# Kernel optimization log

Measured on AMD Instinct MI355X. Metric: run time of the kernel, lower is better.

The kernel has to match this reference:

```python
import jax, jax.numpy as jnp
import numpy as np

LATENT = 3
POLY = 3
SINDY_DIM = 22  # 3 ones + 3 linear + 6 quad + 10 cubic


def sindy_library(z, poly_order=POLY, latent_dim=LATENT):
    # z: [N, latent_dim] -> [N, sindy_dim]; mirrors the torch loop ordering.
    N = z.shape[0]
    cols = [jnp.ones((N,), z.dtype) for _ in range(latent_dim)]
    if poly_order > 0:
        cols += [z[:, i] for i in range(latent_dim)]
    if poly_order > 1:
        for i in range(latent_dim):
            for j in range(i, latent_dim):
                cols.append(z[:, i] * z[:, j])
    if poly_order > 2:
        for i in range(latent_dim):
            for j in range(i, latent_dim):
                for k in range(j, latent_dim):
                    cols.append(z[:, i] * z[:, j] * z[:, k])
    return jnp.stack(cols, axis=1)


def _xavier(key, out_f, in_f):
    lim = np.sqrt(6.0 / (in_f + out_f)).astype(np.float32)
    return jax.random.uniform(key, (out_f, in_f), jnp.float32, -lim, lim)


def setup_inputs() -> dict:
    key = jax.random.key(0)
    ks = jax.random.split(key, 16)
    N, D = 262144, 128
    we = [128, 64, 32, 3]
    wd = [3, 32, 64, 128]
    d = {}
    d["x"] = jax.random.normal(ks[0], (N, D), jnp.float32)
    d["dx"] = jax.random.normal(ks[1], (N, D), jnp.float32)
    for li, (i_f, o_f) in enumerate(zip(we[:-1], we[1:])):
        d[f"We{li+1}"] = _xavier(ks[2 + li], o_f, i_f)
        d[f"be{li+1}"] = jnp.zeros((o_f,), jnp.float32)
    for li, (i_f, o_f) in enumerate(zip(wd[:-1], wd[1:])):
        d[f"Wd{li+1}"] = _xavier(ks[6 + li], o_f, i_f)
        d[f"bd{li+1}"] = jnp.zeros((o_f,), jnp.float32)
    d["EW"] = jnp.full((LATENT, SINDY_DIM), 0.5, jnp.float32)  # nn.init.constant_(E.weight, 0.5)
    d["Eb"] = jax.random.normal(ks[10], (LATENT,), jnp.float32) * 0.1
    return d


def reference(x, dx, We1, be1, We2, be2, We3, be3,
              Wd1, bd1, Wd2, bd2, Wd3, bd3, EW, Eb):
    # encoder forward (Linear + Identity chain)
    z = ((x @ We1.T + be1) @ We2.T + be2) @ We3.T + be3            # [N, L]
    # encoder Jacobian is constant (pure linear chain): J_enc = We3 @ We2 @ We1
    J_enc = We3 @ We2 @ We1                                        # [L, D]
    dz = dx @ J_enc.T                                              # [N, L]
    # SINDy prediction of z-dot
    theta = sindy_library(z)                                       # [N, SINDY_DIM]
    dzb = theta @ EW.T + Eb                                        # [N, L]
    # decoder forward
    xb = ((z @ Wd1.T + bd1) @ Wd2.T + bd2) @ Wd3.T + bd3           # [N, D]
    # decoder Jacobian (constant)
    J_dec = Wd3 @ Wd2 @ Wd1                                        # [D, L]
    dxb = dzb @ J_dec.T                                            # [N, D]
    return z, dz, dzb, xb, dxb
```

## Files before the change

kernel.cpp:

```cpp
#include <hip/hip_runtime.h>

#define D 128

typedef float f32x4 __attribute__((ext_vector_type(4)));

__device__ __forceinline__ float dpp_half_sum(float v) {
    #define DPP_STEP(ctrl, rowmask)                                           \
        v += __int_as_float(__builtin_amdgcn_update_dpp(                      \
                 0, __float_as_int(v), (ctrl), (rowmask), 0xF, true))
    DPP_STEP(0x111, 0xF);
    DPP_STEP(0x112, 0xF);
    DPP_STEP(0x114, 0xF);
    DPP_STEP(0x118, 0xF);
    DPP_STEP(0x142, 0xA);
    #undef DPP_STEP
    return v;
}

__global__ __launch_bounds__(256) void fuse_weights(
    const float* __restrict__ We1, const float* __restrict__ be1,
    const float* __restrict__ We2, const float* __restrict__ be2,
    const float* __restrict__ We3, const float* __restrict__ be3,
    const float* __restrict__ Wd1, const float* __restrict__ bd1,
    const float* __restrict__ Wd2, const float* __restrict__ bd2,
    const float* __restrict__ Wd3, const float* __restrict__ bd3,
    float* __restrict__ ws)
{
    __shared__ float A1[3][64];
    __shared__ float B1[64][3];
    __shared__ float t2d[64];
    const int t = threadIdx.x;

    if (t < 192) {
        {   int r = t >> 6, c = t & 63;
            float s = 0.f;
            #pragma unroll 8
            for (int i = 0; i < 32; ++i) s += We3[r * 32 + i] * We2[i * 64 + c];
            A1[r][c] = s;
        }
        {   int o = t / 3, l = t - o * 3;
            float s = 0.f;
            #pragma unroll 8
            for (int i = 0; i < 32; ++i) s += Wd2[o * 32 + i] * Wd1[i * 3 + l];
            B1[o][l] = s;
        }
    } else {
        int i = t - 192;
        float s = bd2[i];
        #pragma unroll 8
        for (int j = 0; j < 32; ++j) s += Wd2[i * 32 + j] * bd1[j];
        t2d[i] = s;
    }
    __syncthreads();

    for (int e = t; e < 3 * D; e += 256) {
        int r = e >> 7, c = e & 127;
        float s = 0.f;
        #pragma unroll 8
        for (int j = 0; j < 64; ++j) s += A1[r][j] * We1[j * D + c];
        ws[e] = s;
    }
    if (t < 3) {
        float s = be3[t];
        #pragma unroll 8
        for (int j = 0; j < 64; ++j) s += A1[t][j] * be1[j];
        #pragma unroll 8
        for (int i = 0; i < 32; ++i) s += We3[t * 32 + i] * be2[i];
        ws[384 + t] = s;
    }
    if (t < 128) {
        float s0 = 0.f, s1 = 0.f, s2 = 0.f, sb = bd3[t];
        #pragma unroll 8
        for (int j = 0; j < 64; ++j) {
            float w = Wd3[t * 64 + j];
            s0 += w * B1[j][0];
            s1 += w * B1[j][1];
            s2 += w * B1[j][2];
            sb += w * t2d[j];
        }
        ws[512 + t * 4 + 0] = s0;
        ws[512 + t * 4 + 1] = s1;
        ws[512 + t * 4 + 2] = s2;
        ws[512 + t * 4 + 3] = sb;
    }
}

__global__ __launch_bounds__(256) void sindy_all(
    const float* __restrict__ x, const float* __restrict__ dx,
    const float* __restrict__ EW, const float* __restrict__ Eb,
    const float* __restrict__ ws, float* __restrict__ out, int nrows)
{
    __shared__ float sz[768];
    __shared__ float sdz[768];
    __shared__ float sdzb[768];
    __shared__ float sew[69];

    const int t    = threadIdx.x;
    const int lane = t & 31;
    const int half = t >> 5;

    if (t < 66) sew[t] = EW[t];
    else if (t < 69) sew[t] = Eb[t - 66];

    const f32x4 je0 = *((const f32x4*)(ws +   0) + lane);
    const f32x4 je1 = *((const f32x4*)(ws + 128) + lane);
    const f32x4 je2 = *((const f32x4*)(ws + 256) + lane);
    const float benc0 = ws[384], benc1 = ws[385], benc2 = ws[386];
    const f32x4 jd0 = *((const f32x4*)(ws + 512) + lane * 4 + 0);
    const f32x4 jd1 = *((const f32x4*)(ws + 512) + lane * 4 + 1);
    const f32x4 jd2 = *((const f32x4*)(ws + 512) + lane * 4 + 2);
    const f32x4 jd3 = *((const f32x4*)(ws + 512) + lane * 4 + 3);

    const int base = blockIdx.x * 256;
    const int rem  = nrows - base;

    #pragma unroll 4
    for (int i = 0; i < 32; ++i) {
        const int r2  = i * 8 + half;
        const int row = base + r2;
        if (row >= nrows) continue;
        const f32x4 xv = __builtin_nontemporal_load((const f32x4*)(x + (size_t)row * D) + lane);
        float z0 = je0.x*xv.x + je0.y*xv.y + je0.z*xv.z + je0.w*xv.w;
        float z1 = je1.x*xv.x + je1.y*xv.y + je1.z*xv.z + je1.w*xv.w;
        float z2 = je2.x*xv.x + je2.y*xv.y + je2.z*xv.z + je2.w*xv.w;
        z0 = dpp_half_sum(z0);
        z1 = dpp_half_sum(z1);
        z2 = dpp_half_sum(z2);
        if (lane == 31) {
            sz[r2 * 3 + 0] = z0 + benc0;
            sz[r2 * 3 + 1] = z1 + benc1;
            sz[r2 * 3 + 2] = z2 + benc2;
        }
    }

    #pragma unroll 4
    for (int i = 0; i < 32; ++i) {
        const int r2  = i * 8 + half;
        const int row = base + r2;
        if (row >= nrows) continue;
        const f32x4 dv = __builtin_nontemporal_load((const f32x4*)(dx + (size_t)row * D) + lane);
        float d0 = je0.x*dv.x + je0.y*dv.y + je0.z*dv.z + je0.w*dv.w;
        float d1 = je1.x*dv.x + je1.y*dv.y + je1.z*dv.z + je1.w*dv.w;
        float d2 = je2.x*dv.x + je2.y*dv.y + je2.z*dv.z + je2.w*dv.w;
        d0 = dpp_half_sum(d0);
        d1 = dpp_half_sum(d1);
        d2 = dpp_half_sum(d2);
        if (lane == 31) {
            sdz[r2 * 3 + 0] = d0;
            sdz[r2 * 3 + 1] = d1;
            sdz[r2 * 3 + 2] = d2;
        }
    }

    __syncthreads();

    if (t < rem) {
        const float z0 = sz[t * 3 + 0];
        const float z1 = sz[t * 3 + 1];
        const float z2 = sz[t * 3 + 2];

        const float q00 = z0*z0, q01 = z0*z1, q02 = z0*z2;
        const float q11 = z1*z1, q12 = z1*z2, q22 = z2*z2;
        float th[19];
        th[0]=z0;  th[1]=z1;  th[2]=z2;
        th[3]=q00; th[4]=q01; th[5]=q02; th[6]=q11; th[7]=q12; th[8]=q22;
        th[9]=q00*z0;  th[10]=q00*z1; th[11]=q00*z2;
        th[12]=q11*z0; th[13]=q12*z0; th[14]=q22*z0;
        th[15]=q11*z1; th[16]=q11*z2; th[17]=q22*z1; th[18]=q22*z2;

        float b0 = sew[66] + sew[0]  + sew[1]  + sew[2];
        float b1 = sew[67] + sew[22] + sew[23] + sew[24];
        float b2 = sew[68] + sew[44] + sew[45] + sew[46];
        #pragma unroll
        for (int k = 0; k < 19; ++k) {
            b0 += sew[3  + k] * th[k];
            b1 += sew[25 + k] * th[k];
            b2 += sew[47 + k] * th[k];
        }
        sdzb[t * 3 + 0] = b0;
        sdzb[t * 3 + 1] = b1;
        sdzb[t * 3 + 2] = b2;
    }

    __syncthreads();

    if (rem >= 256) {
        if (t < 192) {
            ((f32x4*)(out + (size_t)base * 3))[t]                     = ((const f32x4*)sz)[t];
            ((f32x4*)(out + 3 * (size_t)nrows + (size_t)base * 3))[t] = ((const f32x4*)sdz)[t];
            ((f32x4*)(out + 6 * (size_t)nrows + (size_t)base * 3))[t] = ((const f32x4*)sdzb)[t];
        }
    } else {
        for (int e = t; e < rem * 3; e += 256) {
            out[(size_t)base * 3 + e]                     = sz[e];
            out[3 * (size_t)nrows + (size_t)base * 3 + e] = sdz[e];
            out[6 * (size_t)nrows + (size_t)base * 3 + e] = sdzb[e];
        }
    }

    float* __restrict__ xbout = out + 9 * (size_t)nrows;
    #pragma unroll 4
    for (int i = 0; i < 32; ++i) {
        const int r2  = i * 8 + half;
        const int row = base + r2;
        if (row >= nrows) continue;
        const float z0 = sz[r2 * 3 + 0];
        const float z1 = sz[r2 * 3 + 1];
        const float z2 = sz[r2 * 3 + 2];
        f32x4 v;
        v.x = jd0.x*z0 + jd0.y*z1 + jd0.z*z2 + jd0.w;
        v.y = jd1.x*z0 + jd1.y*z1 + jd1.z*z2 + jd1.w;
        v.z = jd2.x*z0 + jd2.y*z1 + jd2.z*z2 + jd2.w;
        v.w = jd3.x*z0 + jd3.y*z1 + jd3.z*z2 + jd3.w;
        __builtin_nontemporal_store(v, (f32x4*)(xbout + (size_t)row * D) + lane);
    }

    float* __restrict__ dxbout = out + 137 * (size_t)nrows;
    #pragma unroll 4
    for (int i = 0; i < 32; ++i) {
        const int r2  = i * 8 + half;
        const int row = base + r2;
        if (row >= nrows) continue;
        const float b0 = sdzb[r2 * 3 + 0];
        const float b1 = sdzb[r2 * 3 + 1];
        const float b2 = sdzb[r2 * 3 + 2];
        f32x4 v;
        v.x = jd0.x*b0 + jd0.y*b1 + jd0.z*b2;
        v.y = jd1.x*b0 + jd1.y*b1 + jd1.z*b2;
        v.z = jd2.x*b0 + jd2.y*b1 + jd2.z*b2;
        v.w = jd3.x*b0 + jd3.y*b1 + jd3.z*b2;
        __builtin_nontemporal_store(v, (f32x4*)(dxbout + (size_t)row * D) + lane);
    }
}

extern "C" void kernel_launch(void* const* d_in, const int* in_sizes, int n_in,
                              void* d_out, int out_size, void* d_ws, size_t ws_size,
                              hipStream_t stream) {
    const float* x   = (const float*)d_in[0];
    const float* dx  = (const float*)d_in[1];
    const float* We1 = (const float*)d_in[2];
    const float* be1 = (const float*)d_in[3];
    const float* We2 = (const float*)d_in[4];
    const float* be2 = (const float*)d_in[5];
    const float* We3 = (const float*)d_in[6];
    const float* be3 = (const float*)d_in[7];
    const float* Wd1 = (const float*)d_in[8];
    const float* bd1 = (const float*)d_in[9];
    const float* Wd2 = (const float*)d_in[10];
    const float* bd2 = (const float*)d_in[11];
    const float* Wd3 = (const float*)d_in[12];
    const float* bd3 = (const float*)d_in[13];
    const float* EW  = (const float*)d_in[14];
    const float* Eb  = (const float*)d_in[15];

    float* ws  = (float*)d_ws;
    float* out = (float*)d_out;
    const int nrows = in_sizes[0] / D;
    const int nblk  = (nrows + 255) / 256;

    fuse_weights<<<1, 256, 0, stream>>>(We1, be1, We2, be2, We3, be3,
                                        Wd1, bd1, Wd2, bd2, Wd3, bd3, ws);

    sindy_all<<<nblk, 256, 0, stream>>>(x, dx, EW, Eb, ws, out, nrows);
}
```

Measured before the change: 112.8 us.

## Fold weight-fusion kernel into main kernel and drop nontemporal memory hints

Removes the separate single-block fuse_weights launch. Every block of sindy_all now recomputes the fused encoder/decoder Jacobians and biases into shared memory, which avoids one kernel launch and the serialization gap between the two launches. In exchange, each of the 1024 blocks does redundant weight math and reads from the weight arrays (mostly L2 hits) before starting its streaming work. Loads and stores of x, dx, xb and dxb also switch from nontemporal builtins to plain vector accesses.

```diff
diff --git a/kernel.cpp b/kernel.cpp
--- a/kernel.cpp
+++ b/kernel.cpp
@@ -17,99 +17,97 @@
     return v;
 }
 
-__global__ __launch_bounds__(256) void fuse_weights(
+__global__ __launch_bounds__(256) void sindy_all(
+    const float* __restrict__ x, const float* __restrict__ dx,
     const float* __restrict__ We1, const float* __restrict__ be1,
     const float* __restrict__ We2, const float* __restrict__ be2,
     const float* __restrict__ We3, const float* __restrict__ be3,
     const float* __restrict__ Wd1, const float* __restrict__ bd1,
     const float* __restrict__ Wd2, const float* __restrict__ bd2,
     const float* __restrict__ Wd3, const float* __restrict__ bd3,
-    float* __restrict__ ws)
+    const float* __restrict__ EW, const float* __restrict__ Eb,
+    float* __restrict__ out, int nrows)
 {
-    __shared__ float A1[3][64];
-    __shared__ float B1[64][3];
-    __shared__ float t2d[64];
-    const int t = threadIdx.x;
+    __shared__ alignas(16) float A1s[192];
+    __shared__ alignas(16) float B1s[192];
+    __shared__ alignas(16) float t2ds[64];
+    __shared__ alignas(16) float sje[384];
+    __shared__ alignas(16) float sjd[512];
+    __shared__ alignas(16) float sbenc[3];
+    __shared__ alignas(16) float sew[69];
+    __shared__ alignas(16) float sz[768];
+    __shared__ alignas(16) float sdz[768];
+    __shared__ alignas(16) float sdzb[768];
+
+    const int t    = threadIdx.x;
+    const int lane = t & 31;
+    const int half = t >> 5;
 
     if (t < 192) {
         {   int r = t >> 6, c = t & 63;
             float s = 0.f;
             #pragma unroll 8
             for (int i = 0; i < 32; ++i) s += We3[r * 32 + i] * We2[i * 64 + c];
-            A1[r][c] = s;
+            A1s[r * 64 + c] = s;
         }
         {   int o = t / 3, l = t - o * 3;
             float s = 0.f;
             #pragma unroll 8
             for (int i = 0; i < 32; ++i) s += Wd2[o * 32 + i] * Wd1[i * 3 + l];
-            B1[o][l] = s;
+            B1s[o * 3 + l] = s;
         }
     } else {
         int i = t - 192;
         float s = bd2[i];
         #pragma unroll 8
         for (int j = 0; j < 32; ++j) s += Wd2[i * 32 + j] * bd1[j];
-        t2d[i] = s;
-    }
-    __syncthreads();
-
-    for (int e = t; e < 3 * D; e += 256) {
-        int r = e >> 7, c = e & 127;
-        float s = 0.f;
-        #pragma unroll 8
-        for (int j = 0; j < 64; ++j) s += A1[r][j] * We1[j * D + c];
-        ws[e] = s;
-    }
-    if (t < 3) {
-        float s = be3[t];
-        #pragma unroll 8
-        for (int j = 0; j < 64; ++j) s += A1[t][j] * be1[j];
-        #pragma unroll 8
-        for (int i = 0; i < 32; ++i) s += We3[t * 32 + i] * be2[i];
-        ws[384 + t] = s;
-    }
-    if (t < 128) {
-        float s0 = 0.f, s1 = 0.f, s2 = 0.f, sb = bd3[t];
-        #pragma unroll 8
-        for (int j = 0; j < 64; ++j) {
-            float w = Wd3[t * 64 + j];
-            s0 += w * B1[j][0];
-            s1 += w * B1[j][1];
-            s2 += w * B1[j][2];
-            sb += w * t2d[j];
-        }
-        ws[512 + t * 4 + 0] = s0;
-        ws[512 + t * 4 + 1] = s1;
-        ws[512 + t * 4 + 2] = s2;
-        ws[512 + t * 4 + 3] = sb;
-    }
-}
-
-__global__ __launch_bounds__(256) void sindy_all(
-    const float* __restrict__ x, const float* __restrict__ dx,
-    const float* __restrict__ EW, const float* __restrict__ Eb,
-    const float* __restrict__ ws, float* __restrict__ out, int nrows)
-{
-    __shared__ float sz[768];
-    __shared__ float sdz[768];
-    __shared__ float sdzb[768];
-    __shared__ float sew[69];
-
-    const int t    = threadIdx.x;
-    const int lane = t & 31;
-    const int half = t >> 5;
-
-    if (t < 66) sew[t] = EW[t];
-    else if (t < 69) sew[t] = Eb[t - 66];
-
-    const f32x4 je0 = *((const f32x4*)(ws +   0) + lane);
-    const f32x4 je1 = *((const f32x4*)(ws + 128) + lane);
-    const f32x4 je2 = *((const f32x4*)(ws + 256) + lane);
-    const float benc0 = ws[384], benc1 = ws[385], benc2 = ws[386];
-    const f32x4 jd0 = *((const f32x4*)(ws + 512) + lane * 4 + 0);
-    const f32x4 jd1 = *((const f32x4*)(ws + 512) + lane * 4 + 1);
-    const f32x4 jd2 = *((const f32x4*)(ws + 512) + lane * 4 + 2);
-    const f32x4 jd3 = *((const f32x4*)(ws + 512) + lane * 4 + 3);
+        t2ds[i] = s;
+    }
+    if (t < 69) sew[t] = (t < 66) ? EW[t] : Eb[t - 66];
+    __syncthreads();
+
+    {
+        for (int e = t; e < 384; e += 256) {
+            int r = e >> 7, c = e & 127;
+            float s = 0.f;
+            #pragma unroll 8
+            for (int j = 0; j < 64; ++j) s += A1s[r * 64 + j] * We1[j * D + c];
+            sje[e] = s;
+        }
+        if (t < 3) {
+            float s = be3[t];
+            #pragma unroll 8
+            for (int j = 0; j < 64; ++j) s += A1s[t * 64 + j] * be1[j];
+            #pragma unroll 8
+            for (int i = 0; i < 32; ++i) s += We3[t * 32 + i] * be2[i];
+            sbenc[t] = s;
+        }
+        if (t < 128) {
+            float s0 = 0.f, s1 = 0.f, s2 = 0.f, sb = bd3[t];
+            #pragma unroll 8
+            for (int j = 0; j < 64; ++j) {
+                float w = Wd3[t * 64 + j];
+                s0 += w * B1s[j * 3 + 0];
+                s1 += w * B1s[j * 3 + 1];
+                s2 += w * B1s[j * 3 + 2];
+                sb += w * t2ds[j];
+            }
+            sjd[t * 4 + 0] = s0;
+            sjd[t * 4 + 1] = s1;
+            sjd[t * 4 + 2] = s2;
+            sjd[t * 4 + 3] = sb;
+        }
+    }
+    __syncthreads();
+
+    const f32x4 je0 = ((const f32x4*)(sje +   0))[lane];
+    const f32x4 je1 = ((const f32x4*)(sje + 128))[lane];
+    const f32x4 je2 = ((const f32x4*)(sje + 256))[lane];
+    const float benc0 = sbenc[0], benc1 = sbenc[1], benc2 = sbenc[2];
+    const f32x4 jd0 = ((const f32x4*)sjd)[lane * 4 + 0];
+    const f32x4 jd1 = ((const f32x4*)sjd)[lane * 4 + 1];
+    const f32x4 jd2 = ((const f32x4*)sjd)[lane * 4 + 2];
+    const f32x4 jd3 = ((const f32x4*)sjd)[lane * 4 + 3];
 
     const int base = blockIdx.x * 256;
     const int rem  = nrows - base;
@@ -119,7 +117,7 @@
         const int r2  = i * 8 + half;
         const int row = base + r2;
         if (row >= nrows) continue;
-        const f32x4 xv = __builtin_nontemporal_load((const f32x4*)(x + (size_t)row * D) + lane);
+        const f32x4 xv = ((const f32x4*)(x + (size_t)row * D))[lane];
         float z0 = je0.x*xv.x + je0.y*xv.y + je0.z*xv.z + je0.w*xv.w;
         float z1 = je1.x*xv.x + je1.y*xv.y + je1.z*xv.z + je1.w*xv.w;
         float z2 = je2.x*xv.x + je2.y*xv.y + je2.z*xv.z + je2.w*xv.w;
@@ -138,7 +136,7 @@
         const int r2  = i * 8 + half;
         const int row = base + r2;
         if (row >= nrows) continue;
-        const f32x4 dv = __builtin_nontemporal_load((const f32x4*)(dx + (size_t)row * D) + lane);
+        const f32x4 dv = ((const f32x4*)(dx + (size_t)row * D))[lane];
         float d0 = je0.x*dv.x + je0.y*dv.y + je0.z*dv.z + je0.w*dv.w;
         float d1 = je1.x*dv.x + je1.y*dv.y + je1.z*dv.z + je1.w*dv.w;
         float d2 = je2.x*dv.x + je2.y*dv.y + je2.z*dv.z + je2.w*dv.w;
@@ -212,7 +210,7 @@
         v.y = jd1.x*z0 + jd1.y*z1 + jd1.z*z2 + jd1.w;
         v.z = jd2.x*z0 + jd2.y*z1 + jd2.z*z2 + jd2.w;
         v.w = jd3.x*z0 + jd3.y*z1 + jd3.z*z2 + jd3.w;
-        __builtin_nontemporal_store(v, (f32x4*)(xbout + (size_t)row * D) + lane);
+        ((f32x4*)(xbout + (size_t)row * D))[lane] = v;
     }
 
     float* __restrict__ dxbout = out + 137 * (size_t)nrows;
@@ -229,7 +227,7 @@
         v.y = jd1.x*b0 + jd1.y*b1 + jd1.z*b2;
         v.z = jd2.x*b0 + jd2.y*b1 + jd2.z*b2;
         v.w = jd3.x*b0 + jd3.y*b1 + jd3.z*b2;
-        __builtin_nontemporal_store(v, (f32x4*)(dxbout + (size_t)row * D) + lane);
+        ((f32x4*)(dxbout + (size_t)row * D))[lane] = v;
     }
 }
 
@@ -253,13 +251,12 @@
     const float* EW  = (const float*)d_in[14];
     const float* Eb  = (const float*)d_in[15];
 
-    float* ws  = (float*)d_ws;
     float* out = (float*)d_out;
     const int nrows = in_sizes[0] / D;
     const int nblk  = (nrows + 255) / 256;
 
-    fuse_weights<<<1, 256, 0, stream>>>(We1, be1, We2, be2, We3, be3,
-                                        Wd1, bd1, Wd2, bd2, Wd3, bd3, ws);
-
-    sindy_all<<<nblk, 256, 0, stream>>>(x, dx, EW, Eb, ws, out, nrows);
+    sindy_all<<<nblk, 256, 0, stream>>>(x, dx,
+                                        We1, be1, We2, be2, We3, be3,
+                                        Wd1, bd1, Wd2, bd2, Wd3, bd3,
+                                        EW, Eb, out, nrows);
 }
```

New measurement: 142.7 us. +26.5%, slower.
